# Performance work log

Measured on AMD Instinct MI355X. Metric: run time of the kernel, lower is better.

## Reference

```python
import jax, jax.numpy as jnp
import numpy as np

N_NODES = 100000
N_EDGES = 3200000
IN_F, H1, H2, N_CLS = 128, 64, 64, 4


def setup_inputs() -> dict:
    key = jax.random.key(0)
    ks = jax.random.split(key, 8)
    x = jax.random.normal(ks[0], (N_NODES, IN_F), dtype=jnp.float32)
    edge_index = jax.random.randint(ks[1], (2, N_EDGES), 0, N_NODES, dtype=jnp.int32)
    def glorot(k, fan_in, fan_out):
        lim = (6.0 / (fan_in + fan_out)) ** 0.5
        return jax.random.uniform(k, (fan_in, fan_out), jnp.float32, -lim, lim)
    return {
        'x': x,
        'edge_index': edge_index,
        'W1': glorot(ks[2], IN_F, H1), 'b1': jnp.zeros((H1,), jnp.float32),
        'W2': glorot(ks[3], H1, H2),  'b2': jnp.zeros((H2,), jnp.float32),
        'W3': glorot(ks[4], H2, N_CLS), 'b3': jnp.zeros((N_CLS,), jnp.float32),
    }


def gcn_conv(x, row, col, W, b, n_nodes):
    # symmetric normalization D^{-1/2} (A+I) D^{-1/2}, self-loops already in row/col
    deg = jax.ops.segment_sum(jnp.ones_like(col, dtype=x.dtype), col, num_segments=n_nodes)
    dis = jnp.where(deg > 0, jax.lax.rsqrt(jnp.maximum(deg, 1.0)), 0.0)
    norm = dis[row] * dis[col]            # [E']
    h = x @ W                              # [N, out]
    msg = h[row] * norm[:, None]           # gather + scale  [E', out]
    out = jax.ops.segment_sum(msg, col, num_segments=n_nodes)  # scatter-add
    return out + b


def reference(x, edge_index, W1, b1, W2, b2, W3, b3):
    n = x.shape[0]
    loop = jnp.arange(n, dtype=edge_index.dtype)
    row = jnp.concatenate([edge_index[0], loop])
    col = jnp.concatenate([edge_index[1], loop])
    h = gcn_conv(x, row, col, W1, b1, n)
    h = jax.nn.relu(h)
    # dropout p=0.5 is identity in eval mode
    h = gcn_conv(h, row, col, W2, b2, n)
    out = gcn_conv(h, row, col, W3, b3, n)
    return out
```

## Files before the change

kernel.cpp:

```cpp
#include <hip/hip_runtime.h>

#define IN_F 128
#define H 64

#define BKT_BITS 8
#define BKT_SZ 256
#define NBKT_MAX 512
#define CHUNK 8192

using half8 = __attribute__((ext_vector_type(8))) _Float16;
using half4 = __attribute__((ext_vector_type(4))) _Float16;
using f32x4 = __attribute__((ext_vector_type(4))) float;


__global__ void p1_bucket_count(const int* __restrict__ col, int* __restrict__ bucketCnt,
                                int E, int nbkt) {
    __shared__ int h[NBKT_MAX];
    int t = threadIdx.x;
    for (int i = t; i < NBKT_MAX; i += 256) h[i] = 0;
    __syncthreads();
    int beg = blockIdx.x * CHUNK;
    int end = min(E, beg + CHUNK);
    for (int j = beg + t; j < end; j += 256)
        atomicAdd(&h[col[j] >> BKT_BITS], 1);
    __syncthreads();
    for (int i = t; i < nbkt; i += 256)
        if (h[i]) atomicAdd(&bucketCnt[i], h[i]);
}


__global__ void p2_bucket_scan(const int* __restrict__ bucketCnt, int* __restrict__ base,
                               int* __restrict__ cursor, int nbkt) {
    __shared__ int s[NBKT_MAX];
    int t = threadIdx.x;
    int v = (t < nbkt) ? bucketCnt[t] : 0;
    s[t] = v;
    __syncthreads();
    for (int off = 1; off < NBKT_MAX; off <<= 1) {
        int tmp = (t >= off) ? s[t - off] : 0;
        __syncthreads();
        s[t] += tmp;
        __syncthreads();
    }
    if (t < nbkt) {
        int b = s[t] - v;
        base[t] = b;
        cursor[t] = b;
    }
    if (t == nbkt - 1) base[nbkt] = s[t];
}


__global__ void p3_partition(const int* __restrict__ row, const int* __restrict__ col,
                             int* __restrict__ cursor, int* __restrict__ part,
                             int E, int nbkt) {
    __shared__ int h[NBKT_MAX];
    __shared__ int res[NBKT_MAX];
    int t = threadIdx.x;
    for (int i = t; i < NBKT_MAX; i += 256) h[i] = 0;
    __syncthreads();
    int beg = blockIdx.x * CHUNK;
    int end = min(E, beg + CHUNK);
    for (int j = beg + t; j < end; j += 256)
        atomicAdd(&h[col[j] >> BKT_BITS], 1);
    __syncthreads();
    for (int i = t; i < nbkt; i += 256) {
        int c = h[i];
        res[i] = c ? atomicAdd(&cursor[i], c) : 0;
    }
    __syncthreads();
    for (int i = t; i < NBKT_MAX; i += 256) h[i] = 0;
    __syncthreads();
    for (int j = beg + t; j < end; j += 256) {
        int c = col[j];
        int b = c >> BKT_BITS;
        int l = atomicAdd(&h[b], 1);
        int pk = (int)(((unsigned)(c & (BKT_SZ - 1)) << 24) | (unsigned)row[j]);
        part[res[b] + l] = pk;
    }
}


__global__ void p4_csr(const int* __restrict__ part, const int* __restrict__ base,
                       int* __restrict__ offs, int* __restrict__ srcb,
                       float* __restrict__ dis, int N, int nbkt) {
    __shared__ int deg[BKT_SZ];
    __shared__ int lofs[BKT_SZ];
    __shared__ int cur[BKT_SZ];
    int b = blockIdx.x, t = threadIdx.x;
    int eb = base[b], ee = base[b + 1];
    deg[t] = 0;
    __syncthreads();
    for (int j = eb + t; j < ee; j += 256)
        atomicAdd(&deg[(unsigned)part[j] >> 24], 1);
    __syncthreads();
    int v = deg[t];
    lofs[t] = v;
    __syncthreads();
    for (int off = 1; off < BKT_SZ; off <<= 1) {
        int tmp = (t >= off) ? lofs[t - off] : 0;
        __syncthreads();
        lofs[t] += tmp;
        __syncthreads();
    }
    int excl = lofs[t] - v;
    int g = (b << BKT_BITS) + t;
    if (g < N) {
        offs[g] = eb + excl;
        dis[g] = rsqrtf((float)(v + 1));
    }
    if (b == nbkt - 1 && t == 0) offs[N] = ee;
    deg[t] = excl;
    cur[t] = 0;
    __syncthreads();
    for (int j = eb + t; j < ee; j += 256) {
        int pk = part[j];
        int loc = (unsigned)pk >> 24;
        int l = atomicAdd(&cur[loc], 1);
        srcb[eb + deg[loc] + l] = pk & 0xFFFFFF;
    }
}


__global__ void prep_w(const float* __restrict__ W1, const float* __restrict__ W2,
                       _Float16* __restrict__ WT1, _Float16* __restrict__ WT2) {
    int t = blockIdx.x * 256 + threadIdx.x;
    int stride = gridDim.x * 256;
    for (int i = t; i < IN_F * H; i += stride) {
        int k = i >> 6, c = i & 63;
        WT1[c * IN_F + k] = (_Float16)W1[i];
    }
    for (int i = t; i < H * H; i += stride) {
        int k = i >> 6, c = i & 63;
        WT2[c * H + k] = (_Float16)W2[i];
    }
}


__global__ __launch_bounds__(256) void mm1_mfma(const float* __restrict__ x,
                                                const _Float16* __restrict__ WT1,
                                                const float* __restrict__ dis,
                                                _Float16* __restrict__ out, int N) {
    int t = threadIdx.x;
    int w = t >> 6, l = t & 63, lr = l & 15, lg = l >> 4;
    int r0 = blockIdx.x * 64 + w * 16;
    if (r0 >= N) return;
    half8 bfrag[4][4];
#pragma unroll
    for (int ct = 0; ct < 4; ++ct)
#pragma unroll
        for (int ks = 0; ks < 4; ++ks)
            bfrag[ct][ks] = *(const half8*)(WT1 + (size_t)(ct * 16 + lr) * IN_F + ks * 32 + lg * 8);
    int ar = min(r0 + lr, N - 1);
    const float* ap = x + (size_t)ar * IN_F + lg * 8;
    f32x4 acc0 = {0.f, 0.f, 0.f, 0.f}, acc1 = acc0, acc2 = acc0, acc3 = acc0;
#pragma unroll
    for (int ks = 0; ks < 4; ++ks) {
        float4 a0 = *(const float4*)(ap + ks * 32);
        float4 a1 = *(const float4*)(ap + ks * 32 + 4);
        half8 a;
        a[0] = (_Float16)a0.x; a[1] = (_Float16)a0.y; a[2] = (_Float16)a0.z; a[3] = (_Float16)a0.w;
        a[4] = (_Float16)a1.x; a[5] = (_Float16)a1.y; a[6] = (_Float16)a1.z; a[7] = (_Float16)a1.w;
        acc0 = __builtin_amdgcn_mfma_f32_16x16x32_f16(a, bfrag[0][ks], acc0, 0, 0, 0);
        acc1 = __builtin_amdgcn_mfma_f32_16x16x32_f16(a, bfrag[1][ks], acc1, 0, 0, 0);
        acc2 = __builtin_amdgcn_mfma_f32_16x16x32_f16(a, bfrag[2][ks], acc2, 0, 0, 0);
        acc3 = __builtin_amdgcn_mfma_f32_16x16x32_f16(a, bfrag[3][ks], acc3, 0, 0, 0);
    }
#pragma unroll
    for (int reg = 0; reg < 4; ++reg) {
        int r = r0 + lg * 4 + reg;
        if (r < N) {
            float d = dis[r];
            _Float16* o = out + (size_t)r * H + lr;
            o[0]  = (_Float16)(d * acc0[reg]);
            o[16] = (_Float16)(d * acc1[reg]);
            o[32] = (_Float16)(d * acc2[reg]);
            o[48] = (_Float16)(d * acc3[reg]);
        }
    }
}

__global__ __launch_bounds__(256) void mm2_mfma(const _Float16* __restrict__ hh,
                                                const float* __restrict__ b1,
                                                const _Float16* __restrict__ WT2,
                                                const float* __restrict__ dis,
                                                _Float16* __restrict__ out, int N) {
    int t = threadIdx.x;
    int w = t >> 6, l = t & 63, lr = l & 15, lg = l >> 4;
    int r0 = blockIdx.x * 64 + w * 16;
    if (r0 >= N) return;
    half8 bfrag[4][2];
#pragma unroll
    for (int ct = 0; ct < 4; ++ct)
#pragma unroll
        for (int ks = 0; ks < 2; ++ks)
            bfrag[ct][ks] = *(const half8*)(WT2 + (size_t)(ct * 16 + lr) * H + ks * 32 + lg * 8);
    float bias0[8], bias1[8];
#pragma unroll
    for (int j = 0; j < 8; ++j) bias0[j] = b1[lg * 8 + j];
#pragma unroll
    for (int j = 0; j < 8; ++j) bias1[j] = b1[32 + lg * 8 + j];
    int ar = min(r0 + lr, N - 1);
    const _Float16* ap = hh + (size_t)ar * H + lg * 8;
    f32x4 acc0 = {0.f, 0.f, 0.f, 0.f}, acc1 = acc0, acc2 = acc0, acc3 = acc0;
#pragma unroll
    for (int ks = 0; ks < 2; ++ks) {
        half8 a = *(const half8*)(ap + ks * 32);
        half8 af;
#pragma unroll
        for (int j = 0; j < 8; ++j) {
            float v = (float)a[j] + (ks ? bias1[j] : bias0[j]);
            af[j] = (_Float16)fmaxf(v, 0.f);
        }
        acc0 = __builtin_amdgcn_mfma_f32_16x16x32_f16(af, bfrag[0][ks], acc0, 0, 0, 0);
        acc1 = __builtin_amdgcn_mfma_f32_16x16x32_f16(af, bfrag[1][ks], acc1, 0, 0, 0);
        acc2 = __builtin_amdgcn_mfma_f32_16x16x32_f16(af, bfrag[2][ks], acc2, 0, 0, 0);
        acc3 = __builtin_amdgcn_mfma_f32_16x16x32_f16(af, bfrag[3][ks], acc3, 0, 0, 0);
    }
#pragma unroll
    for (int reg = 0; reg < 4; ++reg) {
        int r = r0 + lg * 4 + reg;
        if (r < N) {
            float d = dis[r];
            _Float16* o = out + (size_t)r * H + lr;
            o[0]  = (_Float16)(d * acc0[reg]);
            o[16] = (_Float16)(d * acc1[reg]);
            o[32] = (_Float16)(d * acc2[reg]);
            o[48] = (_Float16)(d * acc3[reg]);
        }
    }
}

__global__ void mm3(const _Float16* __restrict__ hh, const float* __restrict__ b,
                    const float* __restrict__ W, const float* __restrict__ dis,
                    float* __restrict__ out, int N) {
    __shared__ float Wl[H * 4];
    __shared__ float bl[H];
    int t = threadIdx.x;
    if (t < H * 4) Wl[t] = W[t];
    if (t < H) bl[t] = b[t];
    __syncthreads();
    int c = t & 3, rr = t >> 2;
    int r = blockIdx.x * 64 + rr;
    if (r >= N) return;
    const _Float16* h0 = hh + (size_t)r * H;
    float a = 0;
    for (int k = 0; k < H; k += 8) {
        half8 v = *(const half8*)(h0 + k);
#pragma unroll
        for (int j = 0; j < 8; ++j)
            a += ((float)v[j] + bl[k + j]) * Wl[(k + j) * 4 + c];
    }
    out[(size_t)r * 4 + c] = dis[r] * a;
}


__global__ void agg64h(const _Float16* __restrict__ xs, const int* __restrict__ offs,
                       const int* __restrict__ src, const float* __restrict__ dis,
                       _Float16* __restrict__ out, int N) {
    int wid = (blockIdx.x * 256 + threadIdx.x) >> 6;
    int lane = threadIdx.x & 63;
    if (wid >= N) return;
    int s = lane >> 4;
    int f = lane & 15;
    int beg = offs[wid], end = offs[wid + 1];
    int deg = end - beg;
    const _Float16* base = xs + (size_t)f * 4;
    float a0 = 0.f, a1 = 0.f, a2 = 0.f, a3 = 0.f;
    int nfull = deg >> 5;
    int j = beg;
    for (int it = 0; it < nfull; ++it, j += 32) {
        int idx = src[j + (lane & 31)];
#pragma unroll
        for (int k = 0; k < 8; ++k) {
            int sk = __shfl(idx, s * 8 + k);
            half4 v = *(const half4*)(base + (size_t)sk * 64);
            a0 += (float)v[0]; a1 += (float)v[1]; a2 += (float)v[2]; a3 += (float)v[3];
        }
    }
    for (int jj = j + s; jj < end; jj += 4) {
        int sk = src[jj];
        half4 v = *(const half4*)(base + (size_t)sk * 64);
        a0 += (float)v[0]; a1 += (float)v[1]; a2 += (float)v[2]; a3 += (float)v[3];
    }
    a0 += __shfl_xor(a0, 16); a0 += __shfl_xor(a0, 32);
    a1 += __shfl_xor(a1, 16); a1 += __shfl_xor(a1, 32);
    a2 += __shfl_xor(a2, 16); a2 += __shfl_xor(a2, 32);
    a3 += __shfl_xor(a3, 16); a3 += __shfl_xor(a3, 32);
    if (s == 0) {
        half4 sv = *(const half4*)(base + (size_t)wid * 64);
        float d = dis[wid];
        half4 o;
        o[0] = (_Float16)(d * ((float)sv[0] + a0));
        o[1] = (_Float16)(d * ((float)sv[1] + a1));
        o[2] = (_Float16)(d * ((float)sv[2] + a2));
        o[3] = (_Float16)(d * ((float)sv[3] + a3));
        *(half4*)(out + (size_t)wid * 64 + f * 4) = o;
    }
}

__global__ void agg4(const float* __restrict__ xs, const int* __restrict__ offs,
                     const int* __restrict__ src, const float* __restrict__ dis,
                     const float* __restrict__ b, float* __restrict__ out, int N) {
    int i = blockIdx.x * 256 + threadIdx.x;
    if (i >= N) return;
    float4 v = *(const float4*)(xs + (size_t)i * 4);
    float4 acc = v;
    int beg = offs[i], end = offs[i + 1];
    int j = beg;
    for (; j + 3 < end; j += 4) {
        int s0 = src[j], s1 = src[j + 1], s2 = src[j + 2], s3 = src[j + 3];
        float4 m0 = *(const float4*)(xs + (size_t)s0 * 4);
        float4 m1 = *(const float4*)(xs + (size_t)s1 * 4);
        float4 m2 = *(const float4*)(xs + (size_t)s2 * 4);
        float4 m3 = *(const float4*)(xs + (size_t)s3 * 4);
        acc.x += m0.x + m1.x + m2.x + m3.x;
        acc.y += m0.y + m1.y + m2.y + m3.y;
        acc.z += m0.z + m1.z + m2.z + m3.z;
        acc.w += m0.w + m1.w + m2.w + m3.w;
    }
    for (; j < end; ++j) {
        float4 m = *(const float4*)(xs + (size_t)src[j] * 4);
        acc.x += m.x; acc.y += m.y; acc.z += m.z; acc.w += m.w;
    }
    float d = dis[i];
    float4 o;
    o.x = b[0] + d * acc.x;
    o.y = b[1] + d * acc.y;
    o.z = b[2] + d * acc.z;
    o.w = b[3] + d * acc.w;
    *(float4*)(out + (size_t)i * 4) = o;
}


extern "C" void kernel_launch(void* const* d_in, const int* in_sizes, int n_in,
                              void* d_out, int out_size, void* d_ws, size_t ws_size,
                              hipStream_t stream) {
    const float* x  = (const float*)d_in[0];
    const int*   ei = (const int*)d_in[1];
    const float* W1 = (const float*)d_in[2];
    const float* b1 = (const float*)d_in[3];
    const float* W2 = (const float*)d_in[4];
    const float* b2 = (const float*)d_in[5];
    const float* W3 = (const float*)d_in[6];
    const float* b3 = (const float*)d_in[7];
    float* out = (float*)d_out;
    (void)n_in; (void)out_size; (void)ws_size;

    const int N = in_sizes[0] / IN_F;
    const int E = in_sizes[1] / 2;
    const int* row = ei;
    const int* col = ei + E;
    const int nbkt = (N + BKT_SZ - 1) >> BKT_BITS;

    char* w = (char*)d_ws;
    auto carve = [&](size_t bytes) { char* p = w; w += (bytes + 255) & ~(size_t)255; return p; };
    _Float16* bufX  = (_Float16*)carve((size_t)N * H * 2);
    _Float16* bufY  = (_Float16*)carve((size_t)N * H * 2);
    _Float16* WT1   = (_Float16*)carve((size_t)IN_F * H * 2);
    _Float16* WT2   = (_Float16*)carve((size_t)H * H * 2);
    float*  bufC   = (float*)carve((size_t)N * 4 * 4);
    float*  dis    = (float*)carve((size_t)N * 4);
    int*    offs   = (int*)carve((size_t)(N + 1) * 4);
    int*    srcb   = (int*)carve((size_t)E * 4);
    int*    part   = (int*)carve((size_t)E * 4);
    int*    bktCnt = (int*)carve((size_t)NBKT_MAX * 4);
    int*    bktBas = (int*)carve((size_t)(NBKT_MAX + 1) * 4);
    int*    bktCur = (int*)carve((size_t)NBKT_MAX * 4);

    (void)hipMemsetAsync(bktCnt, 0, (size_t)nbkt * 4, stream);

    int gE = (E + CHUNK - 1) / CHUNK;
    int gN = (N + 255) / 256;
    int gMM = (N + 63) / 64;

    p1_bucket_count<<<gE, 256, 0, stream>>>(col, bktCnt, E, nbkt);
    p2_bucket_scan<<<1, NBKT_MAX, 0, stream>>>(bktCnt, bktBas, bktCur, nbkt);
    p3_partition<<<gE, 256, 0, stream>>>(row, col, bktCur, part, E, nbkt);
    p4_csr<<<nbkt, BKT_SZ, 0, stream>>>(part, bktBas, offs, srcb, dis, N, nbkt);

    prep_w<<<48, 256, 0, stream>>>(W1, W2, WT1, WT2);

    mm1_mfma<<<gMM, 256, 0, stream>>>(x, WT1, dis, bufX, N);
    agg64h<<<(N + 3) / 4, 256, 0, stream>>>(bufX, offs, srcb, dis, bufY, N);
    mm2_mfma<<<gMM, 256, 0, stream>>>(bufY, b1, WT2, dis, bufX, N);
    agg64h<<<(N + 3) / 4, 256, 0, stream>>>(bufX, offs, srcb, dis, bufY, N);
    mm3<<<gMM, 256, 0, stream>>>(bufY, b2, W3, dis, bufC, N);
    agg4<<<gN, 256, 0, stream>>>(bufC, offs, srcb, dis, b3, out, N);
}
```

Measured before the change: 310.9 us.

## Split hidden features into quarter planes and aggregate each plane separately

The two dense MFMA kernels now write their fp16 output as four contiguous [N,16] feature planes instead of a row-major [N,64] matrix. The 64-wide aggregation kernel is replaced by a 16-wide kernel launched once per plane. Each pass gathers 32-byte rows from a much smaller table, so the random neighbour gathers should hit in cache more often. In exchange the CSR index array is read four times per layer, there are more kernel launches, and each wave does less work per edge.

Result: slower. 450.8 us (+45.0%).

```diff
diff --git a/kernel.cpp b/kernel.cpp
--- a/kernel.cpp
+++ b/kernel.cpp
@@ -166,16 +166,17 @@
         acc2 = __builtin_amdgcn_mfma_f32_16x16x32_f16(a, bfrag[2][ks], acc2, 0, 0, 0);
         acc3 = __builtin_amdgcn_mfma_f32_16x16x32_f16(a, bfrag[3][ks], acc3, 0, 0, 0);
     }
+    size_t qs = (size_t)N * 16;
 #pragma unroll
     for (int reg = 0; reg < 4; ++reg) {
         int r = r0 + lg * 4 + reg;
         if (r < N) {
             float d = dis[r];
-            _Float16* o = out + (size_t)r * H + lr;
-            o[0]  = (_Float16)(d * acc0[reg]);
-            o[16] = (_Float16)(d * acc1[reg]);
-            o[32] = (_Float16)(d * acc2[reg]);
-            o[48] = (_Float16)(d * acc3[reg]);
+            _Float16* o = out + (size_t)r * 16 + lr;
+            o[0]      = (_Float16)(d * acc0[reg]);
+            o[qs]     = (_Float16)(d * acc1[reg]);
+            o[2 * qs] = (_Float16)(d * acc2[reg]);
+            o[3 * qs] = (_Float16)(d * acc3[reg]);
         }
     }
 }
@@ -217,16 +218,17 @@
         acc2 = __builtin_amdgcn_mfma_f32_16x16x32_f16(af, bfrag[2][ks], acc2, 0, 0, 0);
         acc3 = __builtin_amdgcn_mfma_f32_16x16x32_f16(af, bfrag[3][ks], acc3, 0, 0, 0);
     }
+    size_t qs = (size_t)N * 16;
 #pragma unroll
     for (int reg = 0; reg < 4; ++reg) {
         int r = r0 + lg * 4 + reg;
         if (r < N) {
             float d = dis[r];
-            _Float16* o = out + (size_t)r * H + lr;
-            o[0]  = (_Float16)(d * acc0[reg]);
-            o[16] = (_Float16)(d * acc1[reg]);
-            o[32] = (_Float16)(d * acc2[reg]);
-            o[48] = (_Float16)(d * acc3[reg]);
+            _Float16* o = out + (size_t)r * 16 + lr;
+            o[0]      = (_Float16)(d * acc0[reg]);
+            o[qs]     = (_Float16)(d * acc1[reg]);
+            o[2 * qs] = (_Float16)(d * acc2[reg]);
+            o[3 * qs] = (_Float16)(d * acc3[reg]);
         }
     }
 }
@@ -255,40 +257,49 @@
 }
 
 
-__global__ void agg64h(const _Float16* __restrict__ xs, const int* __restrict__ offs,
-                       const int* __restrict__ src, const float* __restrict__ dis,
-                       _Float16* __restrict__ out, int N) {
+__global__ __launch_bounds__(256) void agg16(const _Float16* __restrict__ xsq,
+                                             const int* __restrict__ offs,
+                                             const int* __restrict__ src,
+                                             const float* __restrict__ dis,
+                                             _Float16* __restrict__ out, int N) {
     int wid = (blockIdx.x * 256 + threadIdx.x) >> 6;
     int lane = threadIdx.x & 63;
     if (wid >= N) return;
-    int s = lane >> 4;
-    int f = lane & 15;
+    int s = lane >> 2;
+    int f = lane & 3;
     int beg = offs[wid], end = offs[wid + 1];
-    int deg = end - beg;
-    const _Float16* base = xs + (size_t)f * 4;
+    const _Float16* base = xsq + (size_t)f * 4;
     float a0 = 0.f, a1 = 0.f, a2 = 0.f, a3 = 0.f;
-    int nfull = deg >> 5;
     int j = beg;
-    for (int it = 0; it < nfull; ++it, j += 32) {
+    for (; j + 31 < end; j += 32) {
         int idx = src[j + (lane & 31)];
-#pragma unroll
-        for (int k = 0; k < 8; ++k) {
-            int sk = __shfl(idx, s * 8 + k);
-            half4 v = *(const half4*)(base + (size_t)sk * 64);
-            a0 += (float)v[0]; a1 += (float)v[1]; a2 += (float)v[2]; a3 += (float)v[3];
-        }
-    }
-    for (int jj = j + s; jj < end; jj += 4) {
+        int s0 = __shfl(idx, s);
+        int s1 = __shfl(idx, s + 16);
+        half4 v0 = *(const half4*)(base + (size_t)s0 * 16);
+        half4 v1 = *(const half4*)(base + (size_t)s1 * 16);
+        a0 += (float)v0[0] + (float)v1[0];
+        a1 += (float)v0[1] + (float)v1[1];
+        a2 += (float)v0[2] + (float)v1[2];
+        a3 += (float)v0[3] + (float)v1[3];
+    }
+    for (; j + 15 < end; j += 16) {
+        int idx = src[j + (lane & 15)];
+        int s0 = __shfl(idx, s);
+        half4 v0 = *(const half4*)(base + (size_t)s0 * 16);
+        a0 += (float)v0[0]; a1 += (float)v0[1]; a2 += (float)v0[2]; a3 += (float)v0[3];
+    }
+    int jj = j + s;
+    if (jj < end) {
         int sk = src[jj];
-        half4 v = *(const half4*)(base + (size_t)sk * 64);
+        half4 v = *(const half4*)(base + (size_t)sk * 16);
         a0 += (float)v[0]; a1 += (float)v[1]; a2 += (float)v[2]; a3 += (float)v[3];
     }
-    a0 += __shfl_xor(a0, 16); a0 += __shfl_xor(a0, 32);
-    a1 += __shfl_xor(a1, 16); a1 += __shfl_xor(a1, 32);
-    a2 += __shfl_xor(a2, 16); a2 += __shfl_xor(a2, 32);
-    a3 += __shfl_xor(a3, 16); a3 += __shfl_xor(a3, 32);
+    a0 += __shfl_xor(a0, 4); a0 += __shfl_xor(a0, 8); a0 += __shfl_xor(a0, 16); a0 += __shfl_xor(a0, 32);
+    a1 += __shfl_xor(a1, 4); a1 += __shfl_xor(a1, 8); a1 += __shfl_xor(a1, 16); a1 += __shfl_xor(a1, 32);
+    a2 += __shfl_xor(a2, 4); a2 += __shfl_xor(a2, 8); a2 += __shfl_xor(a2, 16); a2 += __shfl_xor(a2, 32);
+    a3 += __shfl_xor(a3, 4); a3 += __shfl_xor(a3, 8); a3 += __shfl_xor(a3, 16); a3 += __shfl_xor(a3, 32);
     if (s == 0) {
-        half4 sv = *(const half4*)(base + (size_t)wid * 64);
+        half4 sv = *(const half4*)(base + (size_t)wid * 16);
         float d = dis[wid];
         half4 o;
         o[0] = (_Float16)(d * ((float)sv[0] + a0));
@@ -355,7 +366,7 @@
 
     char* w = (char*)d_ws;
     auto carve = [&](size_t bytes) { char* p = w; w += (bytes + 255) & ~(size_t)255; return p; };
-    _Float16* bufX  = (_Float16*)carve((size_t)N * H * 2);
+    _Float16* bufXq = (_Float16*)carve((size_t)N * H * 2);
     _Float16* bufY  = (_Float16*)carve((size_t)N * H * 2);
     _Float16* WT1   = (_Float16*)carve((size_t)IN_F * H * 2);
     _Float16* WT2   = (_Float16*)carve((size_t)H * H * 2);
@@ -373,6 +384,8 @@
     int gE = (E + CHUNK - 1) / CHUNK;
     int gN = (N + 255) / 256;
     int gMM = (N + 63) / 64;
+    int gAG = (N + 3) / 4;
+    size_t qs = (size_t)N * 16;
 
     p1_bucket_count<<<gE, 256, 0, stream>>>(col, bktCnt, E, nbkt);
     p2_bucket_scan<<<1, NBKT_MAX, 0, stream>>>(bktCnt, bktBas, bktCur, nbkt);
@@ -381,10 +394,12 @@
 
     prep_w<<<48, 256, 0, stream>>>(W1, W2, WT1, WT2);
 
-    mm1_mfma<<<gMM, 256, 0, stream>>>(x, WT1, dis, bufX, N);
-    agg64h<<<(N + 3) / 4, 256, 0, stream>>>(bufX, offs, srcb, dis, bufY, N);
-    mm2_mfma<<<gMM, 256, 0, stream>>>(bufY, b1, WT2, dis, bufX, N);
-    agg64h<<<(N + 3) / 4, 256, 0, stream>>>(bufX, offs, srcb, dis, bufY, N);
+    mm1_mfma<<<gMM, 256, 0, stream>>>(x, WT1, dis, bufXq, N);
+    for (int q = 0; q < 4; ++q)
+        agg16<<<gAG, 256, 0, stream>>>(bufXq + q * qs, offs, srcb, dis, bufY + q * 16, N);
+    mm2_mfma<<<gMM, 256, 0, stream>>>(bufY, b1, WT2, dis, bufXq, N);
+    for (int q = 0; q < 4; ++q)
+        agg16<<<gAG, 256, 0, stream>>>(bufXq + q * qs, offs, srcb, dis, bufY + q * 16, N);
     mm3<<<gMM, 256, 0, stream>>>(bufY, b2, W3, dis, bufC, N);
     agg4<<<gN, 256, 0, stream>>>(bufC, offs, srcb, dis, b3, out, N);
 }
```
